# Performance work log

Hardware: AMD Instinct MI355X
Metric: run time of the kernel (lower is better)

The kernel has to match this reference:

```python
import jax, jax.numpy as jnp
import numpy as np

T, B, D_IN, D_H = 512, 64, 1024, 1024


def setup_inputs() -> dict:
    key = jax.random.key(0)
    ks = jax.random.split(key, 11)
    s = 1.0 / np.sqrt(D_H)
    u = lambda k, shape: jax.random.uniform(k, shape, jnp.float32, -s, s)
    return {
        "emb": jax.random.normal(ks[0], (T, B, D_IN), jnp.float32),
        "hx": jax.random.normal(ks[1], (1, B, D_H), jnp.float32),
        "w_ih_u": u(ks[2], (D_H, D_IN)),
        "w_ih_r": u(ks[3], (D_H, D_IN)),
        "w_ih_c": u(ks[4], (D_H, D_IN)),
        "w_hh_u": u(ks[5], (D_H, D_H)),
        "w_hh_r": u(ks[6], (D_H, D_H)),
        "w_hh_c": u(ks[7], (D_H, D_H)),
        "b_u": u(ks[8], (D_H,)),
        "b_r": u(ks[9], (D_H,)),
        "b_c": u(ks[10], (D_H,)),
    }


def reference(emb, hx, w_ih_u, w_ih_r, w_ih_c, w_hh_u, w_hh_r, w_hh_c, b_u, b_r, b_c):
    # Eval-mode BayesGRU: weight-noise diffs are zero, plain GRU-style recurrence.
    def step(h, x):            # h: [1,B,H], x: [B,D_IN]
        h0 = h[0]              # [B,H]
        upd = jax.nn.sigmoid(x @ w_ih_u.T + h0 @ w_hh_u.T + b_u)
        rst = jax.nn.sigmoid(x @ w_ih_r.T + h0 @ w_hh_r.T + b_r)
        cel = jnp.tanh(x @ w_ih_c.T + (rst * h0) @ w_hh_c.T + b_c)
        hy = (1.0 - upd) * h + upd * cel   # broadcasts to [1,B,H]
        return hy, hy

    hx_final, outs = jax.lax.scan(step, hx, emb)
    outputs = outs.reshape(T, B, D_H)      # torch.cat along dim 0; squeeze(1) no-op for B>1
    return outputs, hx_final
```

## Files before the change

kernel.cpp:

```cpp
#include <hip/hip_runtime.h>
#include <hip/hip_bf16.h>
#include <stdint.h>


#define T_STEPS 512
#define BATCH   64
#define DIN     1024
#define DH      1024
#define NWG     128
#define SLAB    65536

typedef __attribute__((ext_vector_type(8))) short bf16x8;
typedef __attribute__((ext_vector_type(4))) float f32x4;

static __device__ __forceinline__ unsigned short f2bf(float x) {
    union { float f; uint32_t u; } v; v.f = x;
    uint32_t u = v.u;
    return (unsigned short)((u + 0x7FFFu + ((u >> 16) & 1u)) >> 16);
}
static __device__ __forceinline__ float bf2f(unsigned short u) {
    union { uint32_t v; float f; } x; x.v = (uint32_t)u << 16; return x.f;
}
static __device__ __forceinline__ bf16x8 cvt8(float4 a, float4 b) {
    union { bf16x8 v; unsigned d[4]; } u;
    asm("v_cvt_pk_bf16_f32 %0, %1, %2" : "=v"(u.d[0]) : "v"(a.x), "v"(a.y));
    asm("v_cvt_pk_bf16_f32 %0, %1, %2" : "=v"(u.d[1]) : "v"(a.z), "v"(a.w));
    asm("v_cvt_pk_bf16_f32 %0, %1, %2" : "=v"(u.d[2]) : "v"(b.x), "v"(b.y));
    asm("v_cvt_pk_bf16_f32 %0, %1, %2" : "=v"(u.d[3]) : "v"(b.z), "v"(b.w));
    return u.v;
}

static __device__ __forceinline__ int fidx(int row, int k) {
    return ((((row >> 4) * 32 + (k >> 5)) * 64) + (((k >> 3) & 3) * 16) + (row & 15)) * 8
           + (k & 7);
}

static __device__ __forceinline__ void st_wt_u16(void* p, unsigned v) {
    asm volatile("global_store_short %0, %1, off sc0 sc1" :: "v"(p), "v"(v) : "memory");
}
static __device__ __forceinline__ bf16x8 ld_llc(const unsigned short* p) {
    bf16x8 r;
    asm volatile("global_load_dwordx4 %0, %1, off sc0 sc1" : "=v"(r) : "v"(p));
    return r;
}
static __device__ __forceinline__ unsigned ld_llc_u16(const unsigned short* p) {
    unsigned r;
    asm volatile("global_load_ushort %0, %1, off sc0 sc1" : "=v"(r) : "v"(p));
    return r;
}
static __device__ __forceinline__ void vwait0() {
    asm volatile("s_waitcnt vmcnt(0)" ::: "memory");
    __builtin_amdgcn_sched_barrier(0);
}

static __device__ __forceinline__ void wait_fam(const int* cnt, int t, int fam, int quota) {
    const int* b = cnt + t * 128 + fam;
    for (;;) {
        int a0,a1,a2,a3,a4,a5,a6,a7;
        asm volatile("global_load_dword %0, %1, off sc0 sc1" : "=v"(a0) : "v"(b));
        asm volatile("global_load_dword %0, %1, off sc0 sc1" : "=v"(a1) : "v"(b+16));
        asm volatile("global_load_dword %0, %1, off sc0 sc1" : "=v"(a2) : "v"(b+32));
        asm volatile("global_load_dword %0, %1, off sc0 sc1" : "=v"(a3) : "v"(b+48));
        asm volatile("global_load_dword %0, %1, off sc0 sc1" : "=v"(a4) : "v"(b+64));
        asm volatile("global_load_dword %0, %1, off sc0 sc1" : "=v"(a5) : "v"(b+80));
        asm volatile("global_load_dword %0, %1, off sc0 sc1" : "=v"(a6) : "v"(b+96));
        asm volatile("global_load_dword %0, %1, off sc0 sc1" : "=v"(a7) : "v"(b+112));
        asm volatile("s_waitcnt vmcnt(0)" ::: "memory");
        __builtin_amdgcn_sched_barrier(0);
        if (a0>=quota && a1>=quota && a2>=quota && a3>=quota &&
            a4>=quota && a5>=quota && a6>=quota && a7>=quota) break;
        __builtin_amdgcn_s_sleep(1);
    }
}
static __device__ __forceinline__ void wg_wait(const int* cnt, int t, int fam, int quota) {
    if (threadIdx.x == 0) wait_fam(cnt, t, fam, quota);
    __syncthreads();
}
static __device__ __forceinline__ void post_fam(int* cnt, int t, int g, int fam) {
    __hip_atomic_fetch_add(cnt + t * 128 + g * 16 + fam, 1,
                           __ATOMIC_RELAXED, __HIP_MEMORY_SCOPE_AGENT);
}

__global__ __launch_bounds__(256) void gru_pack_weights(
    const float* __restrict__ wihu, const float* __restrict__ wihr,
    const float* __restrict__ wihc, const float* __restrict__ whhu,
    const float* __restrict__ whhr, const float* __restrict__ whhc,
    unsigned short* __restrict__ Wur, unsigned short* __restrict__ Wc)
{
    const int total = 3072 * 2048;
    for (int idx = blockIdx.x * 256 + threadIdx.x; idx < total; idx += gridDim.x * 256) {
        int n = idx >> 11;
        int k = idx & 2047;
        int j = n & 1023;
        float v;
        if (n < 1024)      v = (k < DIN) ? wihu[j*DIN + k] : whhu[j*DH + (k - DIN)];
        else if (n < 2048) v = (k < DIN) ? wihr[j*DIN + k] : whhr[j*DH + (k - DIN)];
        else               v = (k < DIN) ? wihc[j*DIN + k] : whhc[j*DH + (k - DIN)];
        unsigned short bv = f2bf(v);
        int kk = k >> 5, kg = (k >> 3) & 3, r = k & 7;
        if (n < 2048) {
            int b = n >> 4, col = n & 15;
            Wur[((((size_t)kk*128 + b)*4 + kg)*16 + col)*8 + r] = bv;
        } else {
            int nc = n - 2048, b = nc >> 4, col = nc & 15;
            Wc [((((size_t)kk*64 + b)*4 + kg)*16 + col)*8 + r] = bv;
        }
    }
}

__global__ __launch_bounds__(256) void gru_convert_x(
    const float* __restrict__ emb, unsigned short* __restrict__ xbf)
{
    size_t i = (size_t)blockIdx.x * 256 + threadIdx.x;
    float4 v = ((const float4*)emb)[i];
    ushort4 b;
    b.x = f2bf(v.x); b.y = f2bf(v.y); b.z = f2bf(v.z); b.w = f2bf(v.w);
    ((ushort4*)xbf)[i] = b;
}

__global__ __launch_bounds__(256) void gru_init(
    const float* __restrict__ hx, unsigned short* __restrict__ hA,
    int* __restrict__ cnt)
{
    int i = blockIdx.x * 256 + threadIdx.x;
    int row = i >> 10, k = i & 1023;
    hA[fidx(row, k)] = f2bf(hx[i]);
    cnt[i] = 0;
}

__global__ __launch_bounds__(256, 1) void gru_persistent(
    const unsigned short* __restrict__ Wur, const unsigned short* __restrict__ Wc,
    const float* __restrict__ emb, const unsigned short* __restrict__ xbf,
    const float* __restrict__ hx,
    const float* __restrict__ bu, const float* __restrict__ br, const float* __restrict__ bc,
    unsigned short* __restrict__ hA, unsigned short* __restrict__ rh,
    float* __restrict__ out, int* __restrict__ cnt, int deep)
{
    __shared__ unsigned short wur_s[32768];
    __shared__ unsigned short wc_s [32768];

    const int wg   = blockIdx.x;
    const int tid  = threadIdx.x;
    const int lane = tid & 63;
    const int wid  = tid >> 6;
    const int m0   = wid * 16;
    const int c15  = lane & 15;
    const int kg   = lane >> 4;

    for (int i = tid; i < 4096; i += 256) {
        int kk = i >> 6, j = i & 63;
        *((uint4*)wur_s + i) =
            *(const uint4*)((const char*)Wur + ((size_t)kk*128 + wg)*1024 + j*16);
    }
    if (wg < 64) {
        for (int i = tid; i < 4096; i += 256) {
            int kk = i >> 6, j = i & 63;
            *((uint4*)wc_s + i) =
                *(const uint4*)((const char*)Wc + ((size_t)kk*64 + wg)*1024 + j*16);
        }
    }
    __syncthreads();

    const int v    = wg & 63;
    const int colj = v * 16 + c15;

    if (wg < 64) {
        const float bu_ = bu[colj], bc_ = bc[colj];
        float hreg[4];
        #pragma unroll
        for (int i = 0; i < 4; ++i) hreg[i] = hx[(m0 + kg*4 + i) * DH + colj];

        for (int t = 0; t < T_STEPS; ++t) {
            const int par = t & 1;
            const unsigned short* ha   = hA + par * SLAB;
            unsigned short*       hnxt = hA + (par ^ 1) * SLAB;

            f32x4 au = {0.f,0.f,0.f,0.f}, ac = {0.f,0.f,0.f,0.f};
            bf16x8 fr[32];

            if (deep) {
                const unsigned short* xp =
                    xbf + ((size_t)t * BATCH + (m0 + c15)) * DIN + kg * 8;
                #pragma unroll
                for (int kk = 0; kk < 32; ++kk) {
                    bf16x8 f = *(const bf16x8*)(xp + kk * 32);
                    au = __builtin_amdgcn_mfma_f32_16x16x32_bf16(
                             f, *(const bf16x8*)(wur_s + kk*512 + lane*8), au, 0, 0, 0);
                    ac = __builtin_amdgcn_mfma_f32_16x16x32_bf16(
                             f, *(const bf16x8*)(wc_s + kk*512 + lane*8), ac, 0, 0, 0);
                }
            } else {
                const float* xp = emb + ((size_t)t * BATCH + (m0 + c15)) * DIN + kg * 8;
                #pragma unroll
                for (int kk = 0; kk < 32; ++kk) {
                    float4 a = *(const float4*)(xp + kk * 32);
                    float4 b = *(const float4*)(xp + kk * 32 + 4);
                    bf16x8 f = cvt8(a, b);
                    au = __builtin_amdgcn_mfma_f32_16x16x32_bf16(
                             f, *(const bf16x8*)(wur_s + kk*512 + lane*8), au, 0, 0, 0);
                    ac = __builtin_amdgcn_mfma_f32_16x16x32_bf16(
                             f, *(const bf16x8*)(wc_s + kk*512 + lane*8), ac, 0, 0, 0);
                }
            }

            if (t) wg_wait(cnt, t-1, 0, 8);
            const unsigned short* hb = ha + wid * 16384;
            #pragma unroll
            for (int kk = 0; kk < 32; ++kk) fr[kk] = ld_llc(hb + kk * 512 + lane * 8);
            vwait0();
            #pragma unroll
            for (int kk = 0; kk < 32; ++kk)
                au = __builtin_amdgcn_mfma_f32_16x16x32_bf16(
                         fr[kk], *(const bf16x8*)(wur_s + (kk+32)*512 + lane*8), au, 0, 0, 0);

            const unsigned short* rb = rh + wid * 16384;
            wg_wait(cnt, t, 1, 8);
            #pragma unroll
            for (int kk = 0; kk < 32; ++kk) fr[kk] = ld_llc(rb + kk * 512 + lane * 8);

            float ureg[4];
            #pragma unroll
            for (int i = 0; i < 4; ++i)
                ureg[i] = 1.f / (1.f + __expf(-(au[i] + bu_)));

            vwait0();
            #pragma unroll
            for (int kk = 0; kk < 32; ++kk)
                ac = __builtin_amdgcn_mfma_f32_16x16x32_bf16(
                         fr[kk], *(const bf16x8*)(wc_s + (kk+32)*512 + lane*8), ac, 0, 0, 0);

            float hnv[4];
            #pragma unroll
            for (int i = 0; i < 4; ++i) {
                int row = m0 + kg * 4 + i;
                float pre = ac[i] + bc_;
                float e   = __expf(2.f * pre);
                float cel = 1.f - 2.f / (e + 1.f);
                float hn  = (1.f - ureg[i]) * hreg[i] + ureg[i] * cel;
                hreg[i] = hn;
                hnv[i]  = hn;
                st_wt_u16(hnxt + fidx(row, colj), (unsigned)f2bf(hn));
            }
            asm volatile("s_waitcnt vmcnt(0)" ::: "memory");
            __syncthreads();
            if (tid == 0) post_fam(cnt, t, wg >> 3, 0);

            float* out_t = out + (size_t)t * SLAB;
            #pragma unroll
            for (int i = 0; i < 4; ++i) {
                int row = m0 + kg * 4 + i;
                out_t[row * DH + colj] = hnv[i];
                if (t == T_STEPS - 1)
                    out[(size_t)T_STEPS * SLAB + row * DH + colj] = hnv[i];
            }
        }
    } else {
        const float br_ = br[colj];
        for (int t = 0; t < T_STEPS; ++t) {
            const int par = t & 1;
            const unsigned short* ha = hA + par * SLAB;

            f32x4 ar = {0.f,0.f,0.f,0.f};
            bf16x8 fr[32];

            if (deep) {
                const unsigned short* xp =
                    xbf + ((size_t)t * BATCH + (m0 + c15)) * DIN + kg * 8;
                #pragma unroll
                for (int kk = 0; kk < 32; ++kk)
                    ar = __builtin_amdgcn_mfma_f32_16x16x32_bf16(
                             *(const bf16x8*)(xp + kk * 32),
                             *(const bf16x8*)(wur_s + kk*512 + lane*8), ar, 0, 0, 0);
            } else {
                const float* xp = emb + ((size_t)t * BATCH + (m0 + c15)) * DIN + kg * 8;
                #pragma unroll
                for (int kk = 0; kk < 32; ++kk) {
                    float4 a = *(const float4*)(xp + kk * 32);
                    float4 b = *(const float4*)(xp + kk * 32 + 4);
                    ar = __builtin_amdgcn_mfma_f32_16x16x32_bf16(
                             cvt8(a, b), *(const bf16x8*)(wur_s + kk*512 + lane*8),
                             ar, 0, 0, 0);
                }
            }

            if (t) wg_wait(cnt, t-1, 0, 8);
            const unsigned short* hb = ha + wid * 16384;
            unsigned hp16[4];
            #pragma unroll
            for (int i = 0; i < 4; ++i)
                hp16[i] = ld_llc_u16(ha + fidx(m0 + kg*4 + i, colj));
            #pragma unroll
            for (int kk = 0; kk < 32; ++kk) fr[kk] = ld_llc(hb + kk * 512 + lane * 8);
            vwait0();
            #pragma unroll
            for (int kk = 0; kk < 32; ++kk)
                ar = __builtin_amdgcn_mfma_f32_16x16x32_bf16(
                         fr[kk], *(const bf16x8*)(wur_s + (kk+32)*512 + lane*8),
                         ar, 0, 0, 0);

            #pragma unroll
            for (int i = 0; i < 4; ++i) {
                int row = m0 + kg * 4 + i;
                float s = 1.f / (1.f + __expf(-(ar[i] + br_)));
                st_wt_u16(rh + fidx(row, colj),
                          (unsigned)f2bf(s * bf2f((unsigned short)hp16[i])));
            }
            asm volatile("s_waitcnt vmcnt(0)" ::: "memory");
            __syncthreads();
            if (tid == 0) post_fam(cnt, t, v >> 3, 1);
        }
    }
}

extern "C" void kernel_launch(void* const* d_in, const int* in_sizes, int n_in,
                              void* d_out, int out_size, void* d_ws, size_t ws_size,
                              hipStream_t stream)
{
    const float* emb  = (const float*)d_in[0];
    const float* hx   = (const float*)d_in[1];
    const float* wihu = (const float*)d_in[2];
    const float* wihr = (const float*)d_in[3];
    const float* wihc = (const float*)d_in[4];
    const float* whhu = (const float*)d_in[5];
    const float* whhr = (const float*)d_in[6];
    const float* whhc = (const float*)d_in[7];
    const float* bu   = (const float*)d_in[8];
    const float* br   = (const float*)d_in[9];
    const float* bc   = (const float*)d_in[10];
    float* out = (float*)d_out;
    char*  ws  = (char*)d_ws;

    unsigned short* Wur = (unsigned short*)(ws + 0);
    unsigned short* Wc  = (unsigned short*)(ws + 8388608);
    int*            cnt = (int*)(ws + 12582912);
    unsigned short* hA  = (unsigned short*)(ws + 12845056);
    unsigned short* rhb = (unsigned short*)(ws + 13107200);
    unsigned short* xbf = (unsigned short*)(ws + 16777216);
    const int deep = (ws_size >= 83886080ull) ? 1 : 0;

    gru_pack_weights<<<1024, 256, 0, stream>>>(wihu, wihr, wihc, whhu, whhr, whhc, Wur, Wc);
    if (deep) gru_convert_x<<<32768, 256, 0, stream>>>(emb, xbf);
    gru_init<<<256, 256, 0, stream>>>(hx, hA, cnt);
    gru_persistent<<<NWG, 256, 0, stream>>>(Wur, Wc, emb, xbf, hx, bu, br, bc,
                                            hA, rhb, out, cnt, deep);
}
```

Measured before the change: 4.869 ms.

## Use FP8 e4m3 for hidden-state recurrent GEMM in update/reset gates

Adds an FP8 (e4m3) copy of the hidden state and of the recurrent update/reset weights, with the weights scaled by 64. The per-step h @ W_hh products for the update and reset gates now use fp8 MFMA instead of bf16. The goal is to halve the bytes of hidden state each step reads from the LLC and to use faster fp8 MFMA on the latency-critical recurrent path. In exchange it adds an extra byte store of h per step and an fp8 conversion, and it loses accuracy over 512 recurrent steps, which may exceed tolerance.

```diff
diff --git a/kernel.cpp b/kernel.cpp
--- a/kernel.cpp
+++ b/kernel.cpp
@@ -12,6 +12,7 @@
 
 typedef __attribute__((ext_vector_type(8))) short bf16x8;
 typedef __attribute__((ext_vector_type(4))) float f32x4;
+typedef __attribute__((ext_vector_type(2))) int i32x2;
 
 static __device__ __forceinline__ unsigned short f2bf(float x) {
     union { float f; uint32_t u; } v; v.f = x;
@@ -20,6 +21,21 @@
 }
 static __device__ __forceinline__ float bf2f(unsigned short u) {
     union { uint32_t v; float f; } x; x.v = (uint32_t)u << 16; return x.f;
+}
+static __device__ __forceinline__ unsigned char f2e4m3(float x) {
+    union { float f; uint32_t u; } v; v.f = x;
+    unsigned char s = (unsigned char)((v.u >> 24) & 0x80);
+    float ax = fabsf(x);
+    if (ax >= 448.f) return (unsigned char)(s | 0x7e);
+    if (ax < 0.015625f) {
+        int m = (int)(ax * 512.f + 0.5f);
+        return (unsigned char)(s | (unsigned char)m);
+    }
+    uint32_t u = v.u;
+    u += 0x7FFFFu + ((u >> 20) & 1u);
+    int exp = (int)((u >> 23) & 0xff) - 127;
+    uint32_t mant = (u >> 20) & 7u;
+    return (unsigned char)(s | (unsigned char)(((exp + 7) << 3) | mant));
 }
 static __device__ __forceinline__ bf16x8 cvt8(float4 a, float4 b) {
     union { bf16x8 v; unsigned d[4]; } u;
@@ -34,14 +50,26 @@
     return ((((row >> 4) * 32 + (k >> 5)) * 64) + (((k >> 3) & 3) * 16) + (row & 15)) * 8
            + (k & 7);
 }
+static __device__ __forceinline__ int f8idx(int row, int k) {
+    return ((row >> 4) * 32 + (k >> 5)) * 512 + ((k >> 3) & 3) * 128 + (row & 15) * 8
+           + (k & 7);
+}
 
 static __device__ __forceinline__ void st_wt_u16(void* p, unsigned v) {
     asm volatile("global_store_short %0, %1, off sc0 sc1" :: "v"(p), "v"(v) : "memory");
+}
+static __device__ __forceinline__ void st_wt_u8(void* p, unsigned v) {
+    asm volatile("global_store_byte %0, %1, off sc0 sc1" :: "v"(p), "v"(v) : "memory");
 }
 static __device__ __forceinline__ bf16x8 ld_llc(const unsigned short* p) {
     bf16x8 r;
     asm volatile("global_load_dwordx4 %0, %1, off sc0 sc1" : "=v"(r) : "v"(p));
     return r;
+}
+static __device__ __forceinline__ long ld_llc8(const unsigned char* p) {
+    i32x2 r;
+    asm volatile("global_load_dwordx2 %0, %1, off sc0 sc1" : "=v"(r) : "v"(p));
+    union { i32x2 v; long l; } u; u.v = r; return u.l;
 }
 static __device__ __forceinline__ unsigned ld_llc_u16(const unsigned short* p) {
     unsigned r;
@@ -85,7 +113,8 @@
     const float* __restrict__ wihu, const float* __restrict__ wihr,
     const float* __restrict__ wihc, const float* __restrict__ whhu,
     const float* __restrict__ whhr, const float* __restrict__ whhc,
-    unsigned short* __restrict__ Wur, unsigned short* __restrict__ Wc)
+    unsigned short* __restrict__ Wur, unsigned short* __restrict__ Wc,
+    unsigned char* __restrict__ W8, int deep)
 {
     const int total = 3072 * 2048;
     for (int idx = blockIdx.x * 256 + threadIdx.x; idx < total; idx += gridDim.x * 256) {
@@ -101,6 +130,10 @@
         if (n < 2048) {
             int b = n >> 4, col = n & 15;
             Wur[((((size_t)kk*128 + b)*4 + kg)*16 + col)*8 + r] = bv;
+            if (deep && k >= DIN) {
+                int kk8 = kk - 32;
+                W8[(((size_t)kk8*128 + b)*512) + kg*128 + col*8 + r] = f2e4m3(v * 64.f);
+            }
         } else {
             int nc = n - 2048, b = nc >> 4, col = nc & 15;
             Wc [((((size_t)kk*64 + b)*4 + kg)*16 + col)*8 + r] = bv;
@@ -120,24 +153,28 @@
 
 __global__ __launch_bounds__(256) void gru_init(
     const float* __restrict__ hx, unsigned short* __restrict__ hA,
-    int* __restrict__ cnt)
+    unsigned char* __restrict__ hA8, int* __restrict__ cnt)
 {
     int i = blockIdx.x * 256 + threadIdx.x;
     int row = i >> 10, k = i & 1023;
     hA[fidx(row, k)] = f2bf(hx[i]);
+    hA8[f8idx(row, k)] = f2e4m3(hx[i]);
     cnt[i] = 0;
 }
 
 __global__ __launch_bounds__(256, 1) void gru_persistent(
     const unsigned short* __restrict__ Wur, const unsigned short* __restrict__ Wc,
+    const unsigned char* __restrict__ W8,
     const float* __restrict__ emb, const unsigned short* __restrict__ xbf,
     const float* __restrict__ hx,
     const float* __restrict__ bu, const float* __restrict__ br, const float* __restrict__ bc,
-    unsigned short* __restrict__ hA, unsigned short* __restrict__ rh,
+    unsigned short* __restrict__ hA, unsigned char* __restrict__ hA8,
+    unsigned short* __restrict__ rh,
     float* __restrict__ out, int* __restrict__ cnt, int deep)
 {
     __shared__ unsigned short wur_s[32768];
     __shared__ unsigned short wc_s [32768];
+    __shared__ unsigned char  w8_s [16384];
 
     const int wg   = blockIdx.x;
     const int tid  = threadIdx.x;
@@ -147,15 +184,28 @@
     const int c15  = lane & 15;
     const int kg   = lane >> 4;
 
-    for (int i = tid; i < 4096; i += 256) {
-        int kk = i >> 6, j = i & 63;
-        *((uint4*)wur_s + i) =
-            *(const uint4*)((const char*)Wur + ((size_t)kk*128 + wg)*1024 + j*16);
+    if (deep) {
+        for (int i = tid; i < 2048; i += 256) {
+            int kk = i >> 6, j = i & 63;
+            ((uint4*)wur_s)[i] =
+                *(const uint4*)((const char*)Wur + ((size_t)kk*128 + wg)*1024 + j*16);
+        }
+        for (int i = tid; i < 1024; i += 256) {
+            int kk8 = i >> 5, j = i & 31;
+            ((uint4*)w8_s)[i] =
+                *(const uint4*)(W8 + ((size_t)kk8*128 + wg)*512 + j*16);
+        }
+    } else {
+        for (int i = tid; i < 4096; i += 256) {
+            int kk = i >> 6, j = i & 63;
+            ((uint4*)wur_s)[i] =
+                *(const uint4*)((const char*)Wur + ((size_t)kk*128 + wg)*1024 + j*16);
+        }
     }
     if (wg < 64) {
         for (int i = tid; i < 4096; i += 256) {
             int kk = i >> 6, j = i & 63;
-            *((uint4*)wc_s + i) =
+            ((uint4*)wc_s)[i] =
                 *(const uint4*)((const char*)Wc + ((size_t)kk*64 + wg)*1024 + j*16);
         }
     }
@@ -172,10 +222,8 @@
 
         for (int t = 0; t < T_STEPS; ++t) {
             const int par = t & 1;
-            const unsigned short* ha   = hA + par * SLAB;
-            unsigned short*       hnxt = hA + (par ^ 1) * SLAB;
-
             f32x4 au = {0.f,0.f,0.f,0.f}, ac = {0.f,0.f,0.f,0.f};
+            f32x4 au8 = {0.f,0.f,0.f,0.f};
             bf16x8 fr[32];
 
             if (deep) {
@@ -204,14 +252,27 @@
             }
 
             if (t) wg_wait(cnt, t-1, 0, 8);
-            const unsigned short* hb = ha + wid * 16384;
-            #pragma unroll
-            for (int kk = 0; kk < 32; ++kk) fr[kk] = ld_llc(hb + kk * 512 + lane * 8);
-            vwait0();
-            #pragma unroll
-            for (int kk = 0; kk < 32; ++kk)
-                au = __builtin_amdgcn_mfma_f32_16x16x32_bf16(
-                         fr[kk], *(const bf16x8*)(wur_s + (kk+32)*512 + lane*8), au, 0, 0, 0);
+            if (deep) {
+                const unsigned char* hb8 = hA8 + par * SLAB + wid * 16384;
+                long fr8[32];
+                #pragma unroll
+                for (int kk = 0; kk < 32; ++kk) fr8[kk] = ld_llc8(hb8 + kk * 512 + lane * 8);
+                vwait0();
+                #pragma unroll
+                for (int kk = 0; kk < 32; ++kk)
+                    au8 = __builtin_amdgcn_mfma_f32_16x16x32_fp8_fp8(
+                              fr8[kk], *(const long*)(w8_s + kk*512 + lane*8), au8, 0, 0, 0);
+            } else {
+                const unsigned short* hb = hA + par * SLAB + wid * 16384;
+                #pragma unroll
+                for (int kk = 0; kk < 32; ++kk) fr[kk] = ld_llc(hb + kk * 512 + lane * 8);
+                vwait0();
+                #pragma unroll
+                for (int kk = 0; kk < 32; ++kk)
+                    au = __builtin_amdgcn_mfma_f32_16x16x32_bf16(
+                             fr[kk], *(const bf16x8*)(wur_s + (kk+32)*512 + lane*8),
+                             au, 0, 0, 0);
+            }
 
             const unsigned short* rb = rh + wid * 16384;
             wg_wait(cnt, t, 1, 8);
@@ -220,8 +281,10 @@
 
             float ureg[4];
             #pragma unroll
-            for (int i = 0; i < 4; ++i)
-                ureg[i] = 1.f / (1.f + __expf(-(au[i] + bu_)));
+            for (int i = 0; i < 4; ++i) {
+                float pre = au[i] + au8[i] * 0.015625f + bu_;
+                ureg[i] = 1.f / (1.f + __expf(-pre));
+            }
 
             vwait0();
             #pragma unroll
@@ -229,6 +292,8 @@
                 ac = __builtin_amdgcn_mfma_f32_16x16x32_bf16(
                          fr[kk], *(const bf16x8*)(wc_s + (kk+32)*512 + lane*8), ac, 0, 0, 0);
 
+            unsigned short* hnxt  = hA  + (par ^ 1) * SLAB;
+            unsigned char*  hnxt8 = hA8 + (par ^ 1) * SLAB;
             float hnv[4];
             #pragma unroll
             for (int i = 0; i < 4; ++i) {
@@ -240,6 +305,7 @@
                 hreg[i] = hn;
                 hnv[i]  = hn;
                 st_wt_u16(hnxt + fidx(row, colj), (unsigned)f2bf(hn));
+                if (deep) st_wt_u8(hnxt8 + f8idx(row, colj), (unsigned)f2e4m3(hn));
             }
             asm volatile("s_waitcnt vmcnt(0)" ::: "memory");
             __syncthreads();
@@ -261,7 +327,7 @@
             const unsigned short* ha = hA + par * SLAB;
 
             f32x4 ar = {0.f,0.f,0.f,0.f};
-            bf16x8 fr[32];
+            f32x4 ar8 = {0.f,0.f,0.f,0.f};
 
             if (deep) {
                 const unsigned short* xp =
@@ -284,24 +350,38 @@
             }
 
             if (t) wg_wait(cnt, t-1, 0, 8);
-            const unsigned short* hb = ha + wid * 16384;
             unsigned hp16[4];
             #pragma unroll
             for (int i = 0; i < 4; ++i)
                 hp16[i] = ld_llc_u16(ha + fidx(m0 + kg*4 + i, colj));
-            #pragma unroll
-            for (int kk = 0; kk < 32; ++kk) fr[kk] = ld_llc(hb + kk * 512 + lane * 8);
-            vwait0();
-            #pragma unroll
-            for (int kk = 0; kk < 32; ++kk)
-                ar = __builtin_amdgcn_mfma_f32_16x16x32_bf16(
-                         fr[kk], *(const bf16x8*)(wur_s + (kk+32)*512 + lane*8),
-                         ar, 0, 0, 0);
+            if (deep) {
+                const unsigned char* hb8 = hA8 + par * SLAB + wid * 16384;
+                long fr8[32];
+                #pragma unroll
+                for (int kk = 0; kk < 32; ++kk) fr8[kk] = ld_llc8(hb8 + kk * 512 + lane * 8);
+                vwait0();
+                #pragma unroll
+                for (int kk = 0; kk < 32; ++kk)
+                    ar8 = __builtin_amdgcn_mfma_f32_16x16x32_fp8_fp8(
+                              fr8[kk], *(const long*)(w8_s + kk*512 + lane*8), ar8, 0, 0, 0);
+            } else {
+                bf16x8 fr[32];
+                const unsigned short* hb = ha + wid * 16384;
+                #pragma unroll
+                for (int kk = 0; kk < 32; ++kk) fr[kk] = ld_llc(hb + kk * 512 + lane * 8);
+                vwait0();
+                #pragma unroll
+                for (int kk = 0; kk < 32; ++kk)
+                    ar = __builtin_amdgcn_mfma_f32_16x16x32_bf16(
+                             fr[kk], *(const bf16x8*)(wur_s + (kk+32)*512 + lane*8),
+                             ar, 0, 0, 0);
+            }
 
             #pragma unroll
             for (int i = 0; i < 4; ++i) {
                 int row = m0 + kg * 4 + i;
-                float s = 1.f / (1.f + __expf(-(ar[i] + br_)));
+                float pre = ar[i] + ar8[i] * 0.015625f + br_;
+                float s = 1.f / (1.f + __expf(-pre));
                 st_wt_u16(rh + fidx(row, colj),
                           (unsigned)f2bf(s * bf2f((unsigned short)hp16[i])));
             }
@@ -335,12 +415,15 @@
     int*            cnt = (int*)(ws + 12582912);
     unsigned short* hA  = (unsigned short*)(ws + 12845056);
     unsigned short* rhb = (unsigned short*)(ws + 13107200);
+    unsigned char*  hA8 = (unsigned char*)(ws + 13238272);
+    unsigned char*  W8  = (unsigned char*)(ws + 13369344);
     unsigned short* xbf = (unsigned short*)(ws + 16777216);
     const int deep = (ws_size >= 83886080ull) ? 1 : 0;
 
-    gru_pack_weights<<<1024, 256, 0, stream>>>(wihu, wihr, wihc, whhu, whhr, whhc, Wur, Wc);
+    gru_pack_weights<<<1024, 256, 0, stream>>>(wihu, wihr, wihc, whhu, whhr, whhc,
+                                               Wur, Wc, W8, deep);
     if (deep) gru_convert_x<<<32768, 256, 0, stream>>>(emb, xbf);
-    gru_init<<<256, 256, 0, stream>>>(hx, hA, cnt);
-    gru_persistent<<<NWG, 256, 0, stream>>>(Wur, Wc, emb, xbf, hx, bu, br, bc,
-                                            hA, rhb, out, cnt, deep);
-}
+    gru_init<<<256, 256, 0, stream>>>(hx, hA, hA8, cnt);
+    gru_persistent<<<NWG, 256, 0, stream>>>(Wur, Wc, W8, emb, xbf, hx, bu, br, bc,
+                                            hA, hA8, rhb, out, cnt, deep);
+}
```

Result: slower. 5.044 ms (+3.6%).
